# Kernel tuning notes

Hardware: AMD Instinct MI355X
Metric: run time of the kernel (lower is better)

## Reference

```python
import jax, jax.numpy as jnp
import numpy as np

N = 50000          # nodes
E = 800000         # edges (avg degree 16)
IN = 256           # in_feats
H = 8              # num_heads
DH = 32            # out_feats // num_heads
NE = 8             # num_etypes
ALPHA = 0.2        # LeakyReLU slope


def setup_inputs() -> dict:
    key = jax.random.key(0)
    ks = jax.random.split(key, 10)
    feat = jax.random.normal(ks[0], (N, IN), dtype=jnp.float32)
    src = jax.random.randint(ks[1], (E,), 0, N, dtype=jnp.int32)
    dst = jax.random.randint(ks[2], (E,), 0, N, dtype=jnp.int32)
    etype_ids = jax.random.randint(ks[3], (E,), 0, NE, dtype=jnp.int32)
    # learned parameters (xavier-ish scale)
    W_fc = jax.random.normal(ks[4], (IN, H * DH), dtype=jnp.float32) * 0.05
    b_fc = jnp.zeros((H * DH,), dtype=jnp.float32)
    edge_emb = jax.random.normal(ks[5], (NE, H * DH), dtype=jnp.float32) * 0.05
    attn = jax.random.normal(ks[6], (1, H, 3 * DH), dtype=jnp.float32) * 0.05
    W_res = jax.random.normal(ks[7], (IN, H * DH), dtype=jnp.float32) * 0.05
    b_res = jnp.zeros((H * DH,), dtype=jnp.float32)
    return {"feat": feat, "src": src, "dst": dst, "etype_ids": etype_ids,
            "W_fc": W_fc, "b_fc": b_fc, "edge_emb": edge_emb, "attn": attn,
            "W_res": W_res, "b_res": b_res}


def reference(feat, src, dst, etype_ids, W_fc, b_fc, edge_emb, attn, W_res, b_res):
    n = feat.shape[0]
    h = (feat @ W_fc + b_fc).reshape(n, H, DH)            # [N,H,d]
    e = edge_emb[etype_ids].reshape(-1, H, DH)            # [E,H,d]
    # attn dot over concat([h_src, h_dst, e]) decomposes into 3 partial dots
    a_src = attn[0, :, :DH]
    a_dst = attn[0, :, DH:2 * DH]
    a_e = attn[0, :, 2 * DH:]
    s_src = jnp.einsum('nhd,hd->nh', h, a_src)            # [N,H]
    s_dst = jnp.einsum('nhd,hd->nh', h, a_dst)            # [N,H]
    s_e = jnp.einsum('ehd,hd->eh', e, a_e)                # [E,H]
    score = jax.nn.leaky_relu(s_src[src] + s_dst[dst] + s_e, ALPHA)  # [E,H]
    # edge softmax over incoming edges of each dst node
    mx = jax.ops.segment_max(score, dst, num_segments=n)  # [N,H]
    ex = jnp.exp(score - mx[dst])                         # [E,H]
    den = jax.ops.segment_sum(ex, dst, num_segments=n)    # [N,H]
    w = ex / den[dst]                                     # [E,H]
    # scatter-sum weighted source features to destinations
    msg = h[src] * w[:, :, None]                          # [E,H,d]
    out = jax.ops.segment_sum(msg, dst, num_segments=n).reshape(n, H * DH)
    out = out + feat @ W_res + b_res                      # residual
    return jax.nn.elu(out)
```

## Files before the change

### kernel.cpp

```cpp
#include <hip/hip_runtime.h>
#include <hip/hip_bf16.h>
#include <cstdint>

#define NN 50000
#define NEDGE 800000
#define IND 256
#define NH 8
#define DHH 32
#define NET 8
#define LALPHA 0.2f
#define OD 256
#define CD 512
#define SCAN_BLOCKS 196
#define NBG 782
#define NBH 782

typedef __attribute__((ext_vector_type(8))) short short8;
typedef __attribute__((ext_vector_type(4))) float f32x4;
typedef __attribute__((ext_vector_type(4))) float f4v;
typedef __attribute__((ext_vector_type(2))) unsigned u2v;
typedef __attribute__((ext_vector_type(4))) int i4v;

__device__ __forceinline__ unsigned short f2bf(float x) {
  union { float f; unsigned u; } v; v.f = x;
  unsigned r = v.u + 0x7FFFu + ((v.u >> 16) & 1u);
  return (unsigned short)(r >> 16);
}
__device__ __forceinline__ float bf2f(unsigned short u) {
  union { unsigned u; float f; } v; v.u = ((unsigned)u) << 16;
  return v.f;
}
__device__ __forceinline__ float u2f_lo(unsigned w) {
  union { unsigned u; float f; } v; v.u = w << 16; return v.f;
}
__device__ __forceinline__ float u2f_hi(unsigned w) {
  union { unsigned u; float f; } v; v.u = w & 0xffff0000u; return v.f;
}

__global__ __launch_bounds__(256) void k_prep(const float* __restrict__ Wfc,
                                              const float* __restrict__ Wres,
                                              unsigned short* __restrict__ Wtb,
                                              int* __restrict__ cnt,
                                              int* __restrict__ done) {
  int id = blockIdx.x * 256 + threadIdx.x;
  int k = id >> 9;
  int c = id & 511;
  float v = (c < OD) ? Wfc[k * OD + c] : Wres[k * OD + (c - OD)];
  Wtb[(size_t)c * IND + k] = f2bf(v);
  if (id < NN / 4) {
    i4v z = {0, 0, 0, 0};
    *reinterpret_cast<i4v*>(cnt + id * 4) = z;
  }
  if (id == 0) *done = 0;
}

__global__ __launch_bounds__(256, 4) void k_gemm(const float* __restrict__ Af,
                                                 const unsigned short* __restrict__ Bt,
                                                 const float* __restrict__ bfc,
                                                 const float* __restrict__ bres,
                                                 const float* __restrict__ attn,
                                                 const int* __restrict__ dst,
                                                 int* __restrict__ cnt,
                                                 int* __restrict__ rk,
                                                 unsigned short* __restrict__ Hb,
                                                 unsigned short* __restrict__ Rb,
                                                 float* __restrict__ ssrc,
                                                 float* __restrict__ sdst) {
  __shared__ unsigned short Bs[64][272];
  int tid = threadIdx.x;

  if (blockIdx.x >= NBG) {
    int e0 = ((blockIdx.x - NBG) * 256 + tid) << 2;
    if (e0 < NEDGE) {
      i4v d4 = __builtin_nontemporal_load(reinterpret_cast<const i4v*>(dst + e0));
      i4v rv;
      rv.x = atomicAdd(&cnt[d4.x], 1);
      rv.y = atomicAdd(&cnt[d4.y], 1);
      rv.z = atomicAdd(&cnt[d4.z], 1);
      rv.w = atomicAdd(&cnt[d4.w], 1);
      __builtin_nontemporal_store(rv, reinterpret_cast<i4v*>(rk + e0));
    }
    return;
  }

  int wave = tid >> 6, lane = tid & 63;
  int row0 = blockIdx.x * 64;

  int sr = tid >> 2;
  int sc = (tid & 3) * 8;

  int cl = lane & 15;
  int q = lane >> 4;
  int arow = row0 + wave * 16 + cl;
  int lrow = arow < NN ? arow : NN - 1;
  int akof = q * 8;
  short8 areg[8];
#pragma unroll
  for (int ks = 0; ks < 8; ++ks) {
    const float* p = Af + (size_t)lrow * IND + ks * 32 + akof;
    float4 f0 = *reinterpret_cast<const float4*>(p);
    float4 f1 = *reinterpret_cast<const float4*>(p + 4);
    unsigned short t8[8] = {f2bf(f0.x), f2bf(f0.y), f2bf(f0.z), f2bf(f0.w),
                            f2bf(f1.x), f2bf(f1.y), f2bf(f1.z), f2bf(f1.w)};
    areg[ks] = *reinterpret_cast<short8*>(t8);
  }

  for (int bn = 0; bn < 8; ++bn) {
    if (bn) __syncthreads();
#pragma unroll
    for (int j = 0; j < 8; ++j) {
      int k = j * 32 + sc;
      short8 bv = *reinterpret_cast<const short8*>(Bt + (size_t)(bn * 64 + sr) * IND + k);
      *reinterpret_cast<short8*>(&Bs[sr][k]) = bv;
    }
    __syncthreads();

    f32x4 acc[4];
#pragma unroll
    for (int i = 0; i < 4; ++i) acc[i] = (f32x4){0.f, 0.f, 0.f, 0.f};
#pragma unroll
    for (int ks = 0; ks < 8; ++ks) {
#pragma unroll
      for (int nf = 0; nf < 4; ++nf) {
        int colsel = (cl & 12) * 4 + (nf << 2) + (cl & 3);
        short8 b = *reinterpret_cast<const short8*>(&Bs[colsel][ks * 32 + akof]);
        acc[nf] = __builtin_amdgcn_mfma_f32_16x16x32_bf16(b, areg[ks], acc[nf], 0, 0, 0);
      }
    }

    bool isH = (bn < 4);
    int g0 = bn * 64 + q * 16;
    float s0 = 0.f, d0 = 0.f;
    unsigned short o16[16];
    if (isH) {
      int h = bn * 2 + (q >> 1);
      int dd0 = (q & 1) * 16;
#pragma unroll
      for (int nf = 0; nf < 4; ++nf) {
        f4v b4 = *reinterpret_cast<const f4v*>(bfc + g0 + nf * 4);
        f4v as4 = *reinterpret_cast<const f4v*>(attn + h * 96 + dd0 + nf * 4);
        f4v ad4 = *reinterpret_cast<const f4v*>(attn + h * 96 + 32 + dd0 + nf * 4);
#pragma unroll
        for (int r = 0; r < 4; ++r) {
          float val = acc[nf][r] + b4[r];
          o16[nf * 4 + r] = f2bf(val);
          s0 = fmaf(val, as4[r], s0);
          d0 = fmaf(val, ad4[r], d0);
        }
      }
    } else {
#pragma unroll
      for (int nf = 0; nf < 4; ++nf) {
        f4v b4 = *reinterpret_cast<const f4v*>(bres + g0 - 256 + nf * 4);
#pragma unroll
        for (int r = 0; r < 4; ++r) {
          float val = acc[nf][r] + b4[r];
          o16[nf * 4 + r] = f2bf(val);
        }
      }
    }
    if (arow < NN) {
      unsigned short* dp = isH ? (Hb + (size_t)arow * 256 + g0)
                               : (Rb + (size_t)arow * 256 + (g0 - 256));
      *reinterpret_cast<short8*>(dp) = *reinterpret_cast<short8*>(o16);
      *reinterpret_cast<short8*>(dp + 8) = *reinterpret_cast<short8*>(o16 + 8);
    }
    if (isH) {
      s0 += __shfl_xor(s0, 16);
      d0 += __shfl_xor(d0, 16);
      if (!(q & 1) && arow < NN) {
        int h = bn * 2 + (q >> 1);
        ssrc[arow * NH + h] = s0;
        sdst[arow * NH + h] = d0;
      }
    }
  }
}

__global__ __launch_bounds__(256) void k_scanA(const int* __restrict__ cnt,
                                               int* __restrict__ off,
                                               int* __restrict__ bsum,
                                               int* __restrict__ done,
                                               const float* __restrict__ ee,
                                               const float* __restrict__ attn,
                                               float* __restrict__ se,
                                               int* __restrict__ boff) {
  __shared__ int sh[256];
  __shared__ int lastFlag;
  int tid = threadIdx.x;
  int gi = blockIdx.x * 256 + tid;
  int c = (gi < NN) ? cnt[gi] : 0;
  sh[tid] = c;
  __syncthreads();
#pragma unroll
  for (int d = 1; d < 256; d <<= 1) {
    int v = (tid >= d) ? sh[tid - d] : 0;
    __syncthreads();
    sh[tid] += v;
    __syncthreads();
  }
  off[gi] = sh[tid] - c;
  if (tid == 255) {
    bsum[blockIdx.x] = sh[255];
    __threadfence();
    lastFlag = (atomicAdd(done, 1) == SCAN_BLOCKS - 1);
  }
  __syncthreads();
  if (!lastFlag) return;
  __threadfence();
  int cb = (tid < SCAN_BLOCKS)
               ? __hip_atomic_load(&bsum[tid], __ATOMIC_ACQUIRE, __HIP_MEMORY_SCOPE_AGENT)
               : 0;
  __syncthreads();
  sh[tid] = cb;
  __syncthreads();
#pragma unroll
  for (int d = 1; d < 256; d <<= 1) {
    int v = (tid >= d) ? sh[tid - d] : 0;
    __syncthreads();
    sh[tid] += v;
    __syncthreads();
  }
  boff[tid] = sh[tid] - cb;
  int h = tid >> 5, dd = tid & 31;
  float ae = attn[h * 96 + 64 + dd];
  for (int et = 0; et < NET; ++et) {
    float p = ee[et * OD + tid] * ae;
#pragma unroll
    for (int off2 = 16; off2; off2 >>= 1) p += __shfl_xor(p, off2, 32);
    if (dd == 0) se[et * NH + h] = p;
  }
}

__global__ __launch_bounds__(256) void k_scatter(const int* __restrict__ src,
                                                 const int* __restrict__ dst,
                                                 const int* __restrict__ ety,
                                                 const int* __restrict__ rk,
                                                 const int* __restrict__ off,
                                                 const int* __restrict__ boff,
                                                 int* __restrict__ csrp) {
  int t = blockIdx.x * 256 + threadIdx.x;
  int e0 = t << 2;
  if (e0 >= NEDGE) return;
  i4v s4 = __builtin_nontemporal_load(reinterpret_cast<const i4v*>(src + e0));
  i4v d4 = __builtin_nontemporal_load(reinterpret_cast<const i4v*>(dst + e0));
  i4v t4 = __builtin_nontemporal_load(reinterpret_cast<const i4v*>(ety + e0));
  i4v r4 = __builtin_nontemporal_load(reinterpret_cast<const i4v*>(rk + e0));
#pragma unroll
  for (int j = 0; j < 4; ++j) {
    int s = (j == 0) ? s4.x : (j == 1) ? s4.y : (j == 2) ? s4.z : s4.w;
    int d = (j == 0) ? d4.x : (j == 1) ? d4.y : (j == 2) ? d4.z : d4.w;
    int et = (j == 0) ? t4.x : (j == 1) ? t4.y : (j == 2) ? t4.z : t4.w;
    int r = (j == 0) ? r4.x : (j == 1) ? r4.y : (j == 2) ? r4.z : r4.w;
    csrp[off[d] + boff[d >> 8] + r] = (s << 8) | et;
  }
}

__global__ __launch_bounds__(256) void k_edge(const int* __restrict__ csrp,
                                              const float* __restrict__ ssrc,
                                              const float* __restrict__ sdst,
                                              const float* __restrict__ se,
                                              const int* __restrict__ off,
                                              const int* __restrict__ boff,
                                              int* __restrict__ recs) {
  __shared__ float sse[64];
  int tid = threadIdx.x;
  if (tid < 64) sse[tid] = se[tid];
  __syncthreads();
  int v = blockIdx.x * 4 + (tid >> 6);
  int lane = tid & 63;
  int g = lane >> 3, h = lane & 7;
  int lo = off[v] + boff[v >> 8];
  int hi = off[v + 1] + boff[(v + 1) >> 8];
  int n = hi - lo;
  float sd = sdst[v * NH + h];
  for (int i = 0; i < n; i += 8) {
    int idx = i + g;
    bool ok = idx < n;
    int pk = csrp[lo + (ok ? idx : 0)];
    int u = pk >> 8;
    int et = pk & 255;
    float s = ssrc[u * NH + h] + sd + sse[et * NH + h];
    s = s > 0.f ? s : LALPHA * s;
    float p = __expf(s);
    if (ok) {
      int* rp = recs + (size_t)(lo + idx) * 6;
      if (h == 0) rp[0] = u << 8;
      reinterpret_cast<unsigned short*>(rp)[4 + h] = f2bf(p);
    }
  }
}

__global__ __launch_bounds__(256) void k_agg2(const unsigned short* __restrict__ Hb,
                                              const unsigned short* __restrict__ Rb,
                                              const int* __restrict__ off,
                                              const int* __restrict__ boff,
                                              const int* __restrict__ recs,
                                              float* __restrict__ out) {
  int v = blockIdx.x * 4 + (threadIdx.x >> 6);
  int lane = threadIdx.x & 63;
  if (v >= NN) return;
  int h = lane >> 3;
  int lo = off[v] + boff[v >> 8];
  int hi = off[v + 1] + boff[(v + 1) >> 8];
  unsigned lane4 = (unsigned)(lane << 2);
  float a0 = 0.f, a1 = 0.f, a2 = 0.f, a3 = 0.f, dsum = 0.f;
  const int* ri = recs + (size_t)lo * 6;
  const unsigned short* rs = reinterpret_cast<const unsigned short*>(ri);
  int n = hi - lo;
  int i = 0;
  for (; i + 4 <= n; i += 4) {
    unsigned o0 = (unsigned)ri[0] + lane4;
    unsigned o1 = (unsigned)ri[6] + lane4;
    unsigned o2 = (unsigned)ri[12] + lane4;
    unsigned o3 = (unsigned)ri[18] + lane4;
    float p0 = bf2f(rs[4 + h]);
    float p1 = bf2f(rs[16 + h]);
    float p2 = bf2f(rs[28 + h]);
    float p3 = bf2f(rs[40 + h]);
    u2v x0 = *reinterpret_cast<const u2v*>(Hb + o0);
    u2v x1 = *reinterpret_cast<const u2v*>(Hb + o1);
    u2v x2 = *reinterpret_cast<const u2v*>(Hb + o2);
    u2v x3 = *reinterpret_cast<const u2v*>(Hb + o3);
    a0 = fmaf(p0, u2f_lo(x0.x), a0); a1 = fmaf(p0, u2f_hi(x0.x), a1);
    a2 = fmaf(p0, u2f_lo(x0.y), a2); a3 = fmaf(p0, u2f_hi(x0.y), a3);
    a0 = fmaf(p1, u2f_lo(x1.x), a0); a1 = fmaf(p1, u2f_hi(x1.x), a1);
    a2 = fmaf(p1, u2f_lo(x1.y), a2); a3 = fmaf(p1, u2f_hi(x1.y), a3);
    a0 = fmaf(p2, u2f_lo(x2.x), a0); a1 = fmaf(p2, u2f_hi(x2.x), a1);
    a2 = fmaf(p2, u2f_lo(x2.y), a2); a3 = fmaf(p2, u2f_hi(x2.y), a3);
    a0 = fmaf(p3, u2f_lo(x3.x), a0); a1 = fmaf(p3, u2f_hi(x3.x), a1);
    a2 = fmaf(p3, u2f_lo(x3.y), a2); a3 = fmaf(p3, u2f_hi(x3.y), a3);
    dsum += (p0 + p1) + (p2 + p3);
    ri += 24; rs += 48;
  }
  for (; i < n; ++i) {
    unsigned o0 = (unsigned)ri[0] + lane4;
    float p0 = bf2f(rs[4 + h]);
    u2v x0 = *reinterpret_cast<const u2v*>(Hb + o0);
    a0 = fmaf(p0, u2f_lo(x0.x), a0); a1 = fmaf(p0, u2f_hi(x0.x), a1);
    a2 = fmaf(p0, u2f_lo(x0.y), a2); a3 = fmaf(p0, u2f_hi(x0.y), a3);
    dsum += p0;
    ri += 6; rs += 12;
  }
  unsigned oi32 = (unsigned)v * OD + lane4;
  u2v rv = __builtin_nontemporal_load(reinterpret_cast<const u2v*>(Rb + oi32));
  float inv = (dsum > 0.f) ? 1.f / dsum : 0.f;
  float o0 = fmaf(a0, inv, u2f_lo(rv.x));
  float o1 = fmaf(a1, inv, u2f_hi(rv.x));
  float o2 = fmaf(a2, inv, u2f_lo(rv.y));
  float o3 = fmaf(a3, inv, u2f_hi(rv.y));
  f4v wv;
  wv.x = o0 > 0.f ? o0 : expm1f(o0);
  wv.y = o1 > 0.f ? o1 : expm1f(o1);
  wv.z = o2 > 0.f ? o2 : expm1f(o2);
  wv.w = o3 > 0.f ? o3 : expm1f(o3);
  __builtin_nontemporal_store(wv, reinterpret_cast<f4v*>(out + (size_t)v * OD + lane4));
}

extern "C" void kernel_launch(void* const* d_in, const int* in_sizes, int n_in,
                              void* d_out, int out_size, void* d_ws, size_t ws_size,
                              hipStream_t stream) {
  const float* feat = (const float*)d_in[0];
  const int* src = (const int*)d_in[1];
  const int* dst = (const int*)d_in[2];
  const int* ety = (const int*)d_in[3];
  const float* Wfc = (const float*)d_in[4];
  const float* bfc = (const float*)d_in[5];
  const float* ee = (const float*)d_in[6];
  const float* attn = (const float*)d_in[7];
  const float* Wres = (const float*)d_in[8];
  const float* bres = (const float*)d_in[9];
  float* out = (float*)d_out;

  char* w = (char*)d_ws;
  unsigned short* Wtb   = (unsigned short*)w; w += (size_t)CD * IND * 2;
  unsigned short* Hb    = (unsigned short*)w; w += (size_t)NN * OD * 2;
  unsigned short* Rb    = (unsigned short*)w; w += (size_t)NN * OD * 2;
  float* ssrc = (float*)w; w += (size_t)NN * NH * 4;
  float* sdst = (float*)w; w += (size_t)NN * NH * 4;
  float* se   = (float*)w; w += 64 * 4;
  int* cnt    = (int*)w; w += (size_t)NN * 4;
  int* rk     = (int*)w; w += (size_t)NEDGE * 4;
  int* off    = (int*)w; w += (size_t)(SCAN_BLOCKS * 256) * 4;
  int* bsum   = (int*)w; w += 256 * 4;
  int* boff   = (int*)w; w += 256 * 4;
  int* done   = (int*)w; w += 256 * 4;
  int* csrp   = (int*)w; w += (size_t)NEDGE * 4;
  int* recs   = (int*)w; w += (size_t)NEDGE * 24;

  k_prep<<<(CD * IND) / 256, 256, 0, stream>>>(Wfc, Wres, Wtb, cnt, done);
  k_gemm<<<NBG + NBH, 256, 0, stream>>>(feat, Wtb, bfc, bres, attn,
                                        dst, cnt, rk, Hb, Rb, ssrc, sdst);
  k_scanA<<<SCAN_BLOCKS, 256, 0, stream>>>(cnt, off, bsum, done, ee, attn, se, boff);
  k_scatter<<<(NEDGE / 4 + 255) / 256, 256, 0, stream>>>(src, dst, ety, rk,
                                                         off, boff, csrp);
  k_edge<<<NN / 4, 256, 0, stream>>>(csrp, ssrc, sdst, se, off, boff, recs);
  k_agg2<<<NN / 4, 256, 0, stream>>>(Hb, Rb, off, boff, recs, out);
}
```

Before: 181.4 us.

## Fuse edge scoring and aggregation into one kernel using wave shuffles

Merges the edge-score kernel and the aggregation kernel into a single kernel. Each wave computes exp scores for 8 edges across its 8 heads, then broadcasts the scores and source offsets with shuffles while it accumulates the gathered features. This removes the 24-byte-per-edge intermediate record array, along with its global write and read-back and one kernel launch. In exchange, every 8-edge chunk runs the full 8-step inner loop, so low-degree nodes do wasted gather work on padded edges (weighted by zero but still loaded from the row of edge 0), and the gathers are serialized behind shuffles.

New measurement: 168.7 us, median of 2. 1.08x faster.

```diff
diff --git a/kernel.cpp b/kernel.cpp
--- a/kernel.cpp
+++ b/kernel.cpp
@@ -256,91 +256,48 @@
   }
 }
 
-__global__ __launch_bounds__(256) void k_edge(const int* __restrict__ csrp,
+__global__ __launch_bounds__(256) void k_fuse(const unsigned short* __restrict__ Hb,
+                                              const unsigned short* __restrict__ Rb,
+                                              const int* __restrict__ csrp,
                                               const float* __restrict__ ssrc,
                                               const float* __restrict__ sdst,
                                               const float* __restrict__ se,
                                               const int* __restrict__ off,
                                               const int* __restrict__ boff,
-                                              int* __restrict__ recs) {
+                                              float* __restrict__ out) {
   __shared__ float sse[64];
   int tid = threadIdx.x;
   if (tid < 64) sse[tid] = se[tid];
   __syncthreads();
   int v = blockIdx.x * 4 + (tid >> 6);
   int lane = tid & 63;
-  int g = lane >> 3, h = lane & 7;
+  int g = lane >> 3;
+  int hA = lane & 7;
   int lo = off[v] + boff[v >> 8];
   int hi = off[v + 1] + boff[(v + 1) >> 8];
   int n = hi - lo;
-  float sd = sdst[v * NH + h];
+  float sd = sdst[v * NH + hA];
+  unsigned lane4 = (unsigned)(lane << 2);
+  float a0 = 0.f, a1 = 0.f, a2 = 0.f, a3 = 0.f, dsum = 0.f;
   for (int i = 0; i < n; i += 8) {
     int idx = i + g;
     bool ok = idx < n;
     int pk = csrp[lo + (ok ? idx : 0)];
-    int u = pk >> 8;
-    int et = pk & 255;
-    float s = ssrc[u * NH + h] + sd + sse[et * NH + h];
+    int uoff = pk & ~255;
+    float s = ssrc[(pk >> 8) * NH + hA] + sd + sse[((pk & 255) << 3) + hA];
     s = s > 0.f ? s : LALPHA * s;
-    float p = __expf(s);
-    if (ok) {
-      int* rp = recs + (size_t)(lo + idx) * 6;
-      if (h == 0) rp[0] = u << 8;
-      reinterpret_cast<unsigned short*>(rp)[4 + h] = f2bf(p);
-    }
-  }
-}
-
-__global__ __launch_bounds__(256) void k_agg2(const unsigned short* __restrict__ Hb,
-                                              const unsigned short* __restrict__ Rb,
-                                              const int* __restrict__ off,
-                                              const int* __restrict__ boff,
-                                              const int* __restrict__ recs,
-                                              float* __restrict__ out) {
-  int v = blockIdx.x * 4 + (threadIdx.x >> 6);
-  int lane = threadIdx.x & 63;
-  if (v >= NN) return;
-  int h = lane >> 3;
-  int lo = off[v] + boff[v >> 8];
-  int hi = off[v + 1] + boff[(v + 1) >> 8];
-  unsigned lane4 = (unsigned)(lane << 2);
-  float a0 = 0.f, a1 = 0.f, a2 = 0.f, a3 = 0.f, dsum = 0.f;
-  const int* ri = recs + (size_t)lo * 6;
-  const unsigned short* rs = reinterpret_cast<const unsigned short*>(ri);
-  int n = hi - lo;
-  int i = 0;
-  for (; i + 4 <= n; i += 4) {
-    unsigned o0 = (unsigned)ri[0] + lane4;
-    unsigned o1 = (unsigned)ri[6] + lane4;
-    unsigned o2 = (unsigned)ri[12] + lane4;
-    unsigned o3 = (unsigned)ri[18] + lane4;
-    float p0 = bf2f(rs[4 + h]);
-    float p1 = bf2f(rs[16 + h]);
-    float p2 = bf2f(rs[28 + h]);
-    float p3 = bf2f(rs[40 + h]);
-    u2v x0 = *reinterpret_cast<const u2v*>(Hb + o0);
-    u2v x1 = *reinterpret_cast<const u2v*>(Hb + o1);
-    u2v x2 = *reinterpret_cast<const u2v*>(Hb + o2);
-    u2v x3 = *reinterpret_cast<const u2v*>(Hb + o3);
-    a0 = fmaf(p0, u2f_lo(x0.x), a0); a1 = fmaf(p0, u2f_hi(x0.x), a1);
-    a2 = fmaf(p0, u2f_lo(x0.y), a2); a3 = fmaf(p0, u2f_hi(x0.y), a3);
-    a0 = fmaf(p1, u2f_lo(x1.x), a0); a1 = fmaf(p1, u2f_hi(x1.x), a1);
-    a2 = fmaf(p1, u2f_lo(x1.y), a2); a3 = fmaf(p1, u2f_hi(x1.y), a3);
-    a0 = fmaf(p2, u2f_lo(x2.x), a0); a1 = fmaf(p2, u2f_hi(x2.x), a1);
-    a2 = fmaf(p2, u2f_lo(x2.y), a2); a3 = fmaf(p2, u2f_hi(x2.y), a3);
-    a0 = fmaf(p3, u2f_lo(x3.x), a0); a1 = fmaf(p3, u2f_hi(x3.x), a1);
-    a2 = fmaf(p3, u2f_lo(x3.y), a2); a3 = fmaf(p3, u2f_hi(x3.y), a3);
-    dsum += (p0 + p1) + (p2 + p3);
-    ri += 24; rs += 48;
-  }
-  for (; i < n; ++i) {
-    unsigned o0 = (unsigned)ri[0] + lane4;
-    float p0 = bf2f(rs[4 + h]);
-    u2v x0 = *reinterpret_cast<const u2v*>(Hb + o0);
-    a0 = fmaf(p0, u2f_lo(x0.x), a0); a1 = fmaf(p0, u2f_hi(x0.x), a1);
-    a2 = fmaf(p0, u2f_lo(x0.y), a2); a3 = fmaf(p0, u2f_hi(x0.y), a3);
-    dsum += p0;
-    ri += 6; rs += 12;
+    float p = ok ? __expf(s) : 0.f;
+#pragma unroll
+    for (int e = 0; e < 8; ++e) {
+      float pe = __shfl(p, e * 8 + g);
+      unsigned ue = (unsigned)__shfl(uoff, e * 8) + lane4;
+      u2v x = *reinterpret_cast<const u2v*>(Hb + ue);
+      a0 = fmaf(pe, u2f_lo(x.x), a0);
+      a1 = fmaf(pe, u2f_hi(x.x), a1);
+      a2 = fmaf(pe, u2f_lo(x.y), a2);
+      a3 = fmaf(pe, u2f_hi(x.y), a3);
+      dsum += pe;
+    }
   }
   unsigned oi32 = (unsigned)v * OD + lane4;
   u2v rv = __builtin_nontemporal_load(reinterpret_cast<const u2v*>(Rb + oi32));
@@ -386,7 +343,6 @@
   int* boff   = (int*)w; w += 256 * 4;
   int* done   = (int*)w; w += 256 * 4;
   int* csrp   = (int*)w; w += (size_t)NEDGE * 4;
-  int* recs   = (int*)w; w += (size_t)NEDGE * 24;
 
   k_prep<<<(CD * IND) / 256, 256, 0, stream>>>(Wfc, Wres, Wtb, cnt, done);
   k_gemm<<<NBG + NBH, 256, 0, stream>>>(feat, Wtb, bfc, bres, attn,
@@ -394,6 +350,5 @@
   k_scanA<<<SCAN_BLOCKS, 256, 0, stream>>>(cnt, off, bsum, done, ee, attn, se, boff);
   k_scatter<<<(NEDGE / 4 + 255) / 256, 256, 0, stream>>>(src, dst, ety, rk,
                                                          off, boff, csrp);
-  k_edge<<<NN / 4, 256, 0, stream>>>(csrp, ssrc, sdst, se, off, boff, recs);
-  k_agg2<<<NN / 4, 256, 0, stream>>>(Hb, Rb, off, boff, recs, out);
-}
+  k_fuse<<<NN / 4, 256, 0, stream>>>(Hb, Rb, csrp, ssrc, sdst, se, off, boff, out);
+}
```
